# Kernel optimization log

Hardware: AMD Instinct MI355X
Metric: run time of the kernel (lower is better)

Reference implementation:

```python
import jax, jax.numpy as jnp
import numpy as np

GROUP = 128  # GPTQ group size


def _dequant(qweight, qzeros, scales):
    """Dequantize GPTQ int4 packed weights.
    qweight: [K//8, N] int32, 8 nibbles packed along input dim
    qzeros : [G, N//8] int32, 8 nibbles packed along output dim
    scales : [G, N] float
    returns W: [K, N] float, W[r,n] = scales[g,n] * (q[r,n] - (z[g,n]+1)), g = r//GROUP
    """
    shifts = jnp.arange(8, dtype=jnp.int32) * 4
    K8, N = qweight.shape
    # unpack input-dim nibbles: [K//8, 8, N] -> [K, N]
    wi = ((qweight[:, None, :] >> shifts[None, :, None]) & 0xF).reshape(K8 * 8, N)
    # unpack output-dim nibbles: [G, N//8, 8] -> [G, N]
    G = qzeros.shape[0]
    z = ((qzeros[:, :, None] >> shifts[None, None, :]) & 0xF).reshape(G, N)
    g = jnp.arange(K8 * 8) // GROUP  # group index per input row
    return scales[g] * (wi.astype(scales.dtype) - (z[g].astype(scales.dtype) + 1.0))


def setup_inputs() -> dict:
    key = jax.random.key(0)
    k1, k2, k3, k4, k5 = jax.random.split(key, 5)
    B, S, K, N = 4, 32, 4096, 14336
    G = K // GROUP
    x = jax.random.normal(k1, (B, S, K), dtype=jnp.float32)
    qweight = jax.random.randint(k2, (K // 8, N), 0, 2**31 - 1, dtype=jnp.int32)
    qzeros = jax.random.randint(k3, (G, N // 8), 0, 2**31 - 1, dtype=jnp.int32)
    scales = jax.random.uniform(k4, (G, N), dtype=jnp.float32, minval=0.001, maxval=0.02)
    bias = jax.random.normal(k5, (N,), dtype=jnp.float32) * 0.01
    return {"x": x, "qweight": qweight, "qzeros": qzeros, "scales": scales, "bias": bias}


def reference(x, qweight, qzeros, scales, bias):
    # fused dequant + GEMM: out = x @ dequant(W) + bias, shape [B, S, N]
    W = _dequant(qweight, qzeros, scales)
    return x @ W + bias
```

## Files before the change

kernel.cpp:

```cpp
#include <hip/hip_runtime.h>
#include <hip/hip_fp16.h>

typedef _Float16 half8 __attribute__((ext_vector_type(8)));
typedef _Float16 half2v __attribute__((ext_vector_type(2)));
typedef float f32x16 __attribute__((ext_vector_type(16)));

#define BM 128
#define BN 128
#define BK 32
#define THREADS 256
#define LDS_A (BM * BK * 2)
#define LDS_B (BN * BK * 2)
#define LDS_HALF (LDS_A + LDS_B)

__device__ inline unsigned pkrtz(float lo, float hi) {
  return __builtin_bit_cast(unsigned, __builtin_amdgcn_cvt_pkrtz(lo, hi));
}

#define BAR() do { \
  asm volatile("s_waitcnt lgkmcnt(0)" ::: "memory"); \
  __builtin_amdgcn_s_barrier(); \
} while (0)

__global__ void init_out_kernel(const float* __restrict__ bias,
                                float* __restrict__ out, int MN, int N) {
  int i = (blockIdx.x * blockDim.x + threadIdx.x) * 4;
  if (i < MN) *(float4*)(out + i) = *(const float4*)(bias + (i % N));
}

__global__ void reduce_kernel(const float* __restrict__ ws,
                              const float* __restrict__ bias,
                              float* __restrict__ out, int MN, int N, int S) {
  int i = (blockIdx.x * blockDim.x + threadIdx.x) * 4;
  if (i >= MN) return;
  float4 a = *(const float4*)(bias + (i % N));
  for (int z = 0; z < S; ++z) {
    float4 p = *(const float4*)(ws + (size_t)z * MN + i);
    a.x += p.x; a.y += p.y; a.z += p.z; a.w += p.w;
  }
  *(float4*)(out + i) = a;
}

struct Pf {
  float4 a0, a1, a2, a3;
  int w0, w1;
  int zv;
  float s;
};

__global__ __launch_bounds__(THREADS) void qgemm_kernel(
    const float* __restrict__ x, const int* __restrict__ qw,
    const int* __restrict__ qz, const float* __restrict__ sc,
    float* __restrict__ target, int N, int K, int S, int use_ws) {
  __shared__ __align__(16) unsigned char smem[2 * LDS_HALF];
  const int tid = threadIdx.x;
  const int n0 = blockIdx.x * BN;
  const int z = blockIdx.z;
  const int KC = K / S;
  const int kbase = z * KC;
  const int nt = KC / BK;
  const int lane = tid & 63;
  const int wid = tid >> 6;
  const int wr = wid >> 1;
  const int wc = wid & 1;
  const int l31 = lane & 31;
  const int l5 = lane >> 5;
  const int N8 = N >> 3;

  f32x16 acc[2][2] = {};

  const int arow = tid >> 1;
  const int au0 = (tid & 1) * 2;
  const int bcol = tid & 127;
  const int bw0 = (tid >> 7) * 2;
  const int gn = n0 + bcol;

  auto LOAD = [&](int t, Pf& p) {
    int k0 = kbase + t * BK;
    const float* src = x + arow * K + k0 + (tid & 1) * 16;
    p.a0 = *(const float4*)(src);
    p.a1 = *(const float4*)(src + 4);
    p.a2 = *(const float4*)(src + 8);
    p.a3 = *(const float4*)(src + 12);
    int g = k0 >> 7;
    int kq0 = (k0 >> 3) + bw0;
    p.w0 = qw[(kq0 + 0) * N + gn];
    p.w1 = qw[(kq0 + 1) * N + gn];
    p.zv = (qz[g * N8 + (gn >> 3)] >> ((bcol & 7) * 4)) & 0xF;
    p.s = sc[g * N + gn];
  };

  auto STORE = [&](int buf, const Pf& p) {
    unsigned char* base = smem + buf * LDS_HALF;
    uint4 A0, A1;
    A0.x = pkrtz(p.a0.x, p.a1.x);  A0.y = pkrtz(p.a0.y, p.a1.y);
    A0.z = pkrtz(p.a0.z, p.a1.z);  A0.w = pkrtz(p.a0.w, p.a1.w);
    A1.x = pkrtz(p.a2.x, p.a3.x);  A1.y = pkrtz(p.a2.y, p.a3.y);
    A1.z = pkrtz(p.a2.z, p.a3.z);  A1.w = pkrtz(p.a2.w, p.a3.w);
    *(uint4*)(base + arow * 64 + (((au0 + 0) ^ (arow & 3)) << 4)) = A0;
    *(uint4*)(base + arow * 64 + (((au0 + 1) ^ (arow & 3)) << 4)) = A1;

    unsigned char* bb = base + LDS_A;
    unsigned zrep = (0x6400u + (unsigned)p.zv + 1u) * 0x00010001u;
    half2v zh = __builtin_bit_cast(half2v, zrep);
    unsigned srep = pkrtz(p.s, p.s);
    half2v sh = __builtin_bit_cast(half2v, srep);
    const unsigned vw[2] = {(unsigned)p.w0, (unsigned)p.w1};
#pragma unroll
    for (int j = 0; j < 2; ++j) {
      uint4 q;
#pragma unroll
      for (int b = 0; b < 4; ++b) {
        unsigned tt = ((vw[j] >> (4 * b)) & 0x000F000Fu) | 0x64006400u;
        half2v h = (__builtin_bit_cast(half2v, tt) - zh) * sh;
        (&q.x)[b] = __builtin_bit_cast(unsigned, h);
      }
      int u = bw0 + j;
      *(uint4*)(bb + bcol * 64 + ((u ^ (bcol & 3)) << 4)) = q;
    }
  };

  auto COMPUTE = [&](int buf) {
    unsigned char* base = smem + buf * LDS_HALF;
    unsigned char* bb = base + LDS_A;
#pragma unroll
    for (int kk = 0; kk < 2; ++kk) {
      half8 a[2], b[2];
      int u = kk * 2 + l5;
#pragma unroll
      for (int fi = 0; fi < 2; ++fi) {
        int row = wr * 64 + fi * 32 + l31;
        a[fi] = *(half8*)(base + row * 64 + ((u ^ (row & 3)) << 4));
      }
#pragma unroll
      for (int fj = 0; fj < 2; ++fj) {
        int col = wc * 64 + fj * 32 + l31;
        b[fj] = *(half8*)(bb + col * 64 + ((u ^ (col & 3)) << 4));
      }
#pragma unroll
      for (int fi = 0; fi < 2; ++fi)
#pragma unroll
        for (int fj = 0; fj < 2; ++fj)
          acc[fi][fj] = __builtin_amdgcn_mfma_f32_32x32x16_f16(
              a[fi], b[fj], acc[fi][fj], 0, 0, 0);
    }
  };

  Pf sA, sB;
  LOAD(0, sA);
  STORE(0, sA);
  LOAD(1, sB);
  __syncthreads();

  for (int t = 0; t < nt; t += 2) {
    int tA = (t + 2 < nt) ? t + 2 : nt - 1;
    LOAD(tA, sA);
    COMPUTE(0);
    STORE(1, sB);
    BAR();

    int tB = (t + 3 < nt) ? t + 3 : nt - 1;
    LOAD(tB, sB);
    COMPUTE(1);
    STORE(0, sA);
    BAR();
  }

  if (use_ws) {
    float* o = target + (size_t)z * (size_t)BM * N;
#pragma unroll
    for (int fi = 0; fi < 2; ++fi)
#pragma unroll
      for (int fj = 0; fj < 2; ++fj) {
        int gc = n0 + wc * 64 + fj * 32 + l31;
#pragma unroll
        for (int r = 0; r < 16; ++r) {
          int gm = wr * 64 + fi * 32 + (r & 3) + 8 * (r >> 2) + 4 * l5;
          o[(size_t)gm * N + gc] = acc[fi][fj][r];
        }
      }
  } else {
#pragma unroll
    for (int fi = 0; fi < 2; ++fi)
#pragma unroll
      for (int fj = 0; fj < 2; ++fj) {
        int gc = n0 + wc * 64 + fj * 32 + l31;
#pragma unroll
        for (int r = 0; r < 16; ++r) {
          int gm = wr * 64 + fi * 32 + (r & 3) + 8 * (r >> 2) + 4 * l5;
          unsafeAtomicAdd(&target[(size_t)gm * N + gc], acc[fi][fj][r]);
        }
      }
  }
}

extern "C" void kernel_launch(void* const* d_in, const int* in_sizes, int n_in,
                              void* d_out, int out_size, void* d_ws, size_t ws_size,
                              hipStream_t stream) {
  const float* x = (const float*)d_in[0];
  const int* qw = (const int*)d_in[1];
  const int* qz = (const int*)d_in[2];
  const float* sc = (const float*)d_in[3];
  const float* bias = (const float*)d_in[4];
  float* out = (float*)d_out;

  int N = in_sizes[4];
  int K = (in_sizes[1] / N) * 8;
  int M = in_sizes[0] / K;
  int MN = M * N;
  size_t slice = (size_t)MN * 4;

  int S = 0;
  if (ws_size >= 8 * slice) S = 8;
  else if (ws_size >= 4 * slice) S = 4;
  else if (ws_size >= 2 * slice) S = 2;

  if (S > 0) {
    dim3 grid(N / BN, 1, S);
    qgemm_kernel<<<grid, THREADS, 0, stream>>>(x, qw, qz, sc, (float*)d_ws,
                                               N, K, S, 1);
    reduce_kernel<<<(MN / 4 + 255) / 256, 256, 0, stream>>>(
        (const float*)d_ws, bias, out, MN, N, S);
  } else {
    init_out_kernel<<<(MN / 4 + 255) / 256, 256, 0, stream>>>(bias, out, MN, N);
    dim3 grid(N / BN, 1, 8);
    qgemm_kernel<<<grid, THREADS, 0, stream>>>(x, qw, qz, sc, out, N, K, 8, 0);
  }
}
```

Measured before the change: 49.90 us.

## Double BK to 64, single-buffer LDS with one-stage register prefetch

Doubles the K tile to 64 with an 8-way XOR swizzle, removes the LDS double buffer in favour of a single buffer plus a one-deep register prefetch, and adds a launch-bounds occupancy hint of 4 blocks. The intent is fewer loop iterations and barriers per unit of work and more resident blocks for latency hiding. In exchange, compute can no longer overlap the next STORE since both barriers sit around a single buffer, and each thread holds twice as many prefetch registers.

```diff
diff --git a/kernel.cpp b/kernel.cpp
--- a/kernel.cpp
+++ b/kernel.cpp
@@ -7,11 +7,10 @@
 
 #define BM 128
 #define BN 128
-#define BK 32
+#define BK 64
 #define THREADS 256
 #define LDS_A (BM * BK * 2)
 #define LDS_B (BN * BK * 2)
-#define LDS_HALF (LDS_A + LDS_B)
 
 __device__ inline unsigned pkrtz(float lo, float hi) {
   return __builtin_bit_cast(unsigned, __builtin_amdgcn_cvt_pkrtz(lo, hi));
@@ -42,17 +41,17 @@
 }
 
 struct Pf {
-  float4 a0, a1, a2, a3;
-  int w0, w1;
+  float4 a[8];
+  int w0, w1, w2, w3;
   int zv;
   float s;
 };
 
-__global__ __launch_bounds__(THREADS) void qgemm_kernel(
+__global__ __launch_bounds__(THREADS, 4) void qgemm_kernel(
     const float* __restrict__ x, const int* __restrict__ qw,
     const int* __restrict__ qz, const float* __restrict__ sc,
     float* __restrict__ target, int N, int K, int S, int use_ws) {
-  __shared__ __align__(16) unsigned char smem[2 * LDS_HALF];
+  __shared__ __align__(16) unsigned char smem[LDS_A + LDS_B];
   const int tid = threadIdx.x;
   const int n0 = blockIdx.x * BN;
   const int z = blockIdx.z;
@@ -70,44 +69,47 @@
   f32x16 acc[2][2] = {};
 
   const int arow = tid >> 1;
-  const int au0 = (tid & 1) * 2;
+  const int ah = tid & 1;
+  const int au0 = ah * 4;
   const int bcol = tid & 127;
-  const int bw0 = (tid >> 7) * 2;
+  const int brow4 = (tid >> 7) * 4;
   const int gn = n0 + bcol;
 
   auto LOAD = [&](int t, Pf& p) {
     int k0 = kbase + t * BK;
-    const float* src = x + arow * K + k0 + (tid & 1) * 16;
-    p.a0 = *(const float4*)(src);
-    p.a1 = *(const float4*)(src + 4);
-    p.a2 = *(const float4*)(src + 8);
-    p.a3 = *(const float4*)(src + 12);
+    const float* src = x + arow * K + k0 + ah * 32;
+#pragma unroll
+    for (int j = 0; j < 8; ++j) p.a[j] = *(const float4*)(src + 4 * j);
     int g = k0 >> 7;
-    int kq0 = (k0 >> 3) + bw0;
+    int kq0 = (k0 >> 3) + brow4;
     p.w0 = qw[(kq0 + 0) * N + gn];
     p.w1 = qw[(kq0 + 1) * N + gn];
+    p.w2 = qw[(kq0 + 2) * N + gn];
+    p.w3 = qw[(kq0 + 3) * N + gn];
     p.zv = (qz[g * N8 + (gn >> 3)] >> ((bcol & 7) * 4)) & 0xF;
     p.s = sc[g * N + gn];
   };
 
-  auto STORE = [&](int buf, const Pf& p) {
-    unsigned char* base = smem + buf * LDS_HALF;
-    uint4 A0, A1;
-    A0.x = pkrtz(p.a0.x, p.a1.x);  A0.y = pkrtz(p.a0.y, p.a1.y);
-    A0.z = pkrtz(p.a0.z, p.a1.z);  A0.w = pkrtz(p.a0.w, p.a1.w);
-    A1.x = pkrtz(p.a2.x, p.a3.x);  A1.y = pkrtz(p.a2.y, p.a3.y);
-    A1.z = pkrtz(p.a2.z, p.a3.z);  A1.w = pkrtz(p.a2.w, p.a3.w);
-    *(uint4*)(base + arow * 64 + (((au0 + 0) ^ (arow & 3)) << 4)) = A0;
-    *(uint4*)(base + arow * 64 + (((au0 + 1) ^ (arow & 3)) << 4)) = A1;
-
-    unsigned char* bb = base + LDS_A;
+  auto STORE = [&](const Pf& p) {
+#pragma unroll
+    for (int j = 0; j < 4; ++j) {
+      uint4 q;
+      q.x = pkrtz(p.a[2 * j].x, p.a[2 * j + 1].x);
+      q.y = pkrtz(p.a[2 * j].y, p.a[2 * j + 1].y);
+      q.z = pkrtz(p.a[2 * j].z, p.a[2 * j + 1].z);
+      q.w = pkrtz(p.a[2 * j].w, p.a[2 * j + 1].w);
+      int u = au0 + j;
+      *(uint4*)(smem + arow * 128 + ((u ^ (arow & 7)) << 4)) = q;
+    }
+    unsigned char* bb = smem + LDS_A;
     unsigned zrep = (0x6400u + (unsigned)p.zv + 1u) * 0x00010001u;
     half2v zh = __builtin_bit_cast(half2v, zrep);
     unsigned srep = pkrtz(p.s, p.s);
     half2v sh = __builtin_bit_cast(half2v, srep);
-    const unsigned vw[2] = {(unsigned)p.w0, (unsigned)p.w1};
-#pragma unroll
-    for (int j = 0; j < 2; ++j) {
+    const unsigned vw[4] = {(unsigned)p.w0, (unsigned)p.w1,
+                            (unsigned)p.w2, (unsigned)p.w3};
+#pragma unroll
+    for (int j = 0; j < 4; ++j) {
       uint4 q;
 #pragma unroll
       for (int b = 0; b < 4; ++b) {
@@ -115,27 +117,26 @@
         half2v h = (__builtin_bit_cast(half2v, tt) - zh) * sh;
         (&q.x)[b] = __builtin_bit_cast(unsigned, h);
       }
-      int u = bw0 + j;
-      *(uint4*)(bb + bcol * 64 + ((u ^ (bcol & 3)) << 4)) = q;
+      int u = brow4 + j;
+      *(uint4*)(bb + bcol * 128 + ((u ^ (bcol & 7)) << 4)) = q;
     }
   };
 
-  auto COMPUTE = [&](int buf) {
-    unsigned char* base = smem + buf * LDS_HALF;
-    unsigned char* bb = base + LDS_A;
-#pragma unroll
-    for (int kk = 0; kk < 2; ++kk) {
+  auto COMPUTE = [&]() {
+    unsigned char* bb = smem + LDS_A;
+#pragma unroll
+    for (int kk = 0; kk < 4; ++kk) {
       half8 a[2], b[2];
       int u = kk * 2 + l5;
 #pragma unroll
       for (int fi = 0; fi < 2; ++fi) {
         int row = wr * 64 + fi * 32 + l31;
-        a[fi] = *(half8*)(base + row * 64 + ((u ^ (row & 3)) << 4));
+        a[fi] = *(half8*)(smem + row * 128 + ((u ^ (row & 7)) << 4));
       }
 #pragma unroll
       for (int fj = 0; fj < 2; ++fj) {
         int col = wc * 64 + fj * 32 + l31;
-        b[fj] = *(half8*)(bb + col * 64 + ((u ^ (col & 3)) << 4));
+        b[fj] = *(half8*)(bb + col * 128 + ((u ^ (col & 7)) << 4));
       }
 #pragma unroll
       for (int fi = 0; fi < 2; ++fi)
@@ -146,24 +147,14 @@
     }
   };
 
-  Pf sA, sB;
-  LOAD(0, sA);
-  STORE(0, sA);
-  LOAD(1, sB);
-  __syncthreads();
-
-  for (int t = 0; t < nt; t += 2) {
-    int tA = (t + 2 < nt) ? t + 2 : nt - 1;
-    LOAD(tA, sA);
-    COMPUTE(0);
-    STORE(1, sB);
+  Pf p;
+  LOAD(0, p);
+  for (int t = 0; t < nt; ++t) {
     BAR();
-
-    int tB = (t + 3 < nt) ? t + 3 : nt - 1;
-    LOAD(tB, sB);
-    COMPUTE(1);
-    STORE(0, sA);
+    STORE(p);
+    if (t + 1 < nt) LOAD(t + 1, p);
     BAR();
+    COMPUTE();
   }
 
   if (use_ws) {
```

New measurement: 69.85 us. 1.4x slower.
